# Kernel optimization log

Hardware: AMD Instinct MI355X
Metric: run time of the kernel (lower is better)

The kernel has to match this reference:

```python
import jax, jax.numpy as jnp
import numpy as np

DIM, HEADS, HEAD_DIM = 1024, 16, 64
B, S = 2, 1024
LAMBDA = 4.0
EPS = 1e-6


def setup_inputs() -> dict:
    key = jax.random.key(0)
    ks = jax.random.split(key, 7)
    sc = 1.0 / np.sqrt(DIM)
    return {
        "x": jax.random.normal(ks[0], (B, S, DIM), jnp.float32),
        "qkv_w": jax.random.normal(ks[1], (3 * DIM, DIM), jnp.float32) * sc,
        "qkv_b": jax.random.normal(ks[2], (3 * DIM,), jnp.float32) * 0.01,
        "proj_w": jax.random.normal(ks[3], (DIM, DIM), jnp.float32) * sc,
        "proj_b": jax.random.normal(ks[4], (DIM,), jnp.float32) * 0.01,
        "dwc_w": jax.random.normal(ks[5], (DIM, 1, 3), jnp.float32) * 0.3,
        "dwc_b": jax.random.normal(ks[6], (DIM,), jnp.float32) * 0.01,
    }


def _l1_dist(q, k):
    # q,k: [B,H,S,Dh] -> pairwise L1 distance [B,H,S,S].
    # Accumulate over head_dim with a (rematerialized) scan so we never
    # materialize the [B,H,S,S,Dh] broadcast tensor.
    qT = jnp.moveaxis(q, -1, 0)  # [Dh,B,H,S]
    kT = jnp.moveaxis(k, -1, 0)

    def step(acc, qk):
        qd, kd = qk  # [B,H,S]
        return acc + jnp.abs(qd[..., :, None] - kd[..., None, :]), None

    init = jnp.zeros(q.shape[:-1] + (k.shape[-2],), q.dtype)
    dist, _ = jax.lax.scan(jax.checkpoint(step), init, (qT, kT))
    return dist


def reference(x, qkv_w, qkv_b, proj_w, proj_b, dwc_w, dwc_b):
    Bq, Sq, C = x.shape
    # qkv projection -> q,k,v each [B,H,S,Dh]
    qkv = (x @ qkv_w.T + qkv_b).reshape(Bq, Sq, 3, HEADS, HEAD_DIM)
    qkv = jnp.transpose(qkv, (2, 0, 3, 1, 4))
    q, k, v = qkv[0], qkv[1], qkv[2]

    # exact Laplacian (L1-distance) kernel attention, row-normalized
    dist = _l1_dist(q, k)                       # [B,H,S,S]
    kern = jnp.exp(-LAMBDA * dist / HEAD_DIM)   # mean-L1 scaling
    attn = kern / (jnp.sum(kern, axis=-1, keepdims=True) + EPS)
    global_attn = jnp.einsum("bhij,bhjd->bhid", attn, v)

    # depthwise conv1d local branch on v (channel order = head-major)
    v1d = jnp.transpose(v, (0, 1, 3, 2)).reshape(Bq, C, Sq)  # [B,C,S]
    local = jax.lax.conv_general_dilated(
        v1d, dwc_w, window_strides=(1,), padding=((1, 1),),
        feature_group_count=C, dimension_numbers=("NCH", "OIH", "NCH"))
    local = local + dwc_b[None, :, None]
    local = jnp.transpose(local.reshape(Bq, HEADS, HEAD_DIM, Sq), (0, 1, 3, 2))

    y = global_attn + local                      # [B,H,S,Dh]
    y = jnp.transpose(y, (0, 2, 1, 3)).reshape(Bq, Sq, C)
    return y @ proj_w.T + proj_b
```

## Files before the change

### kernel.cpp

```cpp
#include <hip/hip_runtime.h>

#define DIMC 1024
#define HEADS 16
#define HD 64
#define BATCH 2
#define SEQ 1024
#define NQKV 3072

typedef _Float16 f16;
typedef _Float16 half8 __attribute__((ext_vector_type(8)));
typedef _Float16 half4v __attribute__((ext_vector_type(4)));
typedef float floatx4 __attribute__((ext_vector_type(4)));

__device__ __forceinline__ void gld16(const void* g, void* l) {
  __builtin_amdgcn_global_load_lds((const __attribute__((address_space(1))) void*)g,
                                   (__attribute__((address_space(3))) void*)l, 16, 0, 0);
}

__device__ __forceinline__ unsigned sadU8(unsigned a, unsigned b, unsigned c) {
#if __has_builtin(__builtin_amdgcn_sad_u8)
  return __builtin_amdgcn_sad_u8(a, b, c);
#else
  unsigned d;
  asm("v_sad_u8 %0, %1, %2, %3" : "=v"(d) : "v"(a), "v"(b), "v"(c));
  return d;
#endif
}

__global__ __launch_bounds__(256) void cvt_kernel(
    const float* __restrict__ x, const float* __restrict__ wq, const float* __restrict__ wp,
    f16* __restrict__ x16, f16* __restrict__ wq16, f16* __restrict__ wp16)
{
  int bid = blockIdx.x;
  const float* src; f16* dst; int base;
  if (bid < 512)        { src = x;  dst = x16;  base = bid; }
  else if (bid < 1280)  { src = wq; dst = wq16; base = bid - 512; }
  else                  { src = wp; dst = wp16; base = bid - 1280; }
  long long i0 = (long long)base*1024 + threadIdx.x;
#pragma unroll
  for (int k2 = 0; k2 < 4; ++k2) {
    long long i = i0 + k2*256;
    float4 v = ((const float4*)src)[i];
    half4v h; h[0]=(f16)v.x; h[1]=(f16)v.y; h[2]=(f16)v.z; h[3]=(f16)v.w;
    *(half4v*)(dst + i*4) = h;
  }
}

template<int TM, int TN, int BK, int MW, int MODE>
__global__ __launch_bounds__(256, MW) void gemm_kernel(
    const f16* __restrict__ A, const f16* __restrict__ Bw, const float* __restrict__ bias,
    unsigned char* __restrict__ q8, unsigned char* __restrict__ k8, f16* __restrict__ vT,
    float* __restrict__ outp, int K)
{
  constexpr int MT = TM / 32;
  constexpr int NT = TN / 32;
  constexpr int G  = BK / 8;
  __shared__ f16 As[TM*BK];
  __shared__ f16 Bs[TN*BK];
  const int tid = threadIdx.x;
  const int wave = tid >> 6, lane = tid & 63;
  const int lq = lane >> 4, li = lane & 15;
  const int m0 = blockIdx.y * TM, n0 = blockIdx.x * TN;
  const int wm = (wave & 1) * (TM/2), wn = (wave >> 1) * (TN/2);
  floatx4 acc[MT][NT] = {};

  const int kIters = K / BK;
  for (int kt = 0; kt < kIters; ++kt) {
    __syncthreads();
#pragma unroll
    for (int r = 0; r < TM*BK/2048; ++r) {
      int slot = r*256 + tid;
      int row = slot / G, c = slot % G, g = c ^ (row & (G-1));
      gld16(A + (size_t)(m0+row)*K + kt*BK + g*8, As + slot*8);
    }
#pragma unroll
    for (int r = 0; r < TN*BK/2048; ++r) {
      int slot = r*256 + tid;
      int row = slot / G, c = slot % G, g = c ^ (row & (G-1));
      gld16(Bw + (size_t)(n0+row)*K + kt*BK + g*8, Bs + slot*8);
    }
    __syncthreads();
#pragma unroll
    for (int ks = 0; ks < BK/32; ++ks) {
      half8 af[MT], bf[NT];
      int kc = ks*4 + lq;
#pragma unroll
      for (int t = 0; t < MT; ++t) {
        int am = wm + t*16 + li;
        af[t] = *(const half8*)&As[am*BK + (kc ^ (am & (G-1)))*8];
      }
#pragma unroll
      for (int t = 0; t < NT; ++t) {
        int bn = wn + t*16 + li;
        bf[t] = *(const half8*)&Bs[bn*BK + (kc ^ (bn & (G-1)))*8];
      }
#pragma unroll
      for (int mt = 0; mt < MT; ++mt)
#pragma unroll
        for (int nt = 0; nt < NT; ++nt)
          acc[mt][nt] = __builtin_amdgcn_mfma_f32_16x16x32_f16(af[mt], bf[nt], acc[mt][nt], 0, 0, 0);
    }
  }

#pragma unroll
  for (int mt = 0; mt < MT; ++mt) {
#pragma unroll
    for (int nt = 0; nt < NT; ++nt) {
      int f = n0 + wn + nt*16 + li;
      float bb = bias[f];
      if (MODE == 0) {
        int which = f >> 10, cc = f & 1023, h = cc >> 6, d = cc & 63;
        int t0 = m0 + wm + mt*16 + lq*4;
        int b = t0 >> 10, s0 = t0 & 1023;
        if (which == 2) {
          half4v hv;
#pragma unroll
          for (int r = 0; r < 4; ++r) hv[r] = (f16)(acc[mt][nt][r] + bb);
          *(half4v*)&vT[((size_t)((b*HEADS + h)*HD + d))*SEQ + s0] = hv;
        } else {
          unsigned char* dst = (which == 0) ? q8 : k8;
#pragma unroll
          for (int r = 0; r < 4; ++r) {
            float v = acc[mt][nt][r] + bb;
            int u = (int)floorf(v * 16.0f + 128.5f);
            u = u < 0 ? 0 : (u > 255 ? 255 : u);
            dst[((size_t)((b*HEADS + h)*SEQ + s0 + r))*HD + d] = (unsigned char)u;
          }
        }
      } else {
#pragma unroll
        for (int r = 0; r < 4; ++r) {
          int t = m0 + wm + mt*16 + lq*4 + r;
          outp[(size_t)t*DIMC + f] = acc[mt][nt][r] + bb;
        }
      }
    }
  }
}

__global__ __launch_bounds__(256, 4) void attn_kernel(
    const unsigned char* __restrict__ q8g, const unsigned char* __restrict__ k8g,
    const f16* __restrict__ vTg, const float* __restrict__ dwcw, const float* __restrict__ dwcb,
    f16* __restrict__ y16)
{
  __shared__ unsigned char q8s[32*64];
  __shared__ unsigned char k8s[2][128*64];
  __shared__ f16 sfrag[2][8*64*8];
  __shared__ float rspart[32*16];
  __shared__ float rowsum[32];

  const int tid = threadIdx.x;
  const int lin = blockIdx.x + 16 * blockIdx.y;
  const int bh = (lin & 7) * 4 + ((lin >> 3) & 3);
  const int i0 = (lin >> 5) * 32;
  const int lane = tid & 63, wave = tid >> 6;
  const int lq = lane >> 4, li = lane & 15;
  const int iL = tid & 15, jt = tid >> 4;
  const int ksj = jt >> 2, qj = jt & 3;
  const int scs = jt & 3;

  {
    if (tid < 128)
      gld16(q8g + ((size_t)(bh*SEQ) + i0)*HD + tid*16, q8s + tid*16);
#pragma unroll
    for (int r = 0; r < 2; ++r) {
      int slot = r*256 + tid;
      int row = slot >> 2, c4 = slot & 3, sc4 = c4 ^ ((row >> 3) & 3);
      gld16(k8g + ((size_t)(bh*SEQ) + row)*HD + sc4*16, k8s[0] + slot*16);
    }
  }
  __syncthreads();

  unsigned qr[2][16];
#pragma unroll
  for (int n = 0; n < 2; ++n)
#pragma unroll
    for (int c4 = 0; c4 < 4; ++c4) {
      uint4 t = *(const uint4*)&q8s[(iL + n*16)*64 + c4*16];
      qr[n][c4*4+0] = t.x; qr[n][c4*4+1] = t.y; qr[n][c4*4+2] = t.z; qr[n][c4*4+3] = t.w;
    }

  float rs[2] = {0.f, 0.f};
  floatx4 pacc[2] = {};
  const f16* vbase = vTg + ((size_t)(bh*HD) + wave*16 + li)*SEQ;

  for (int jb = 0; jb < 8; ++jb) {
    const int j0 = jb * 128;
    const int cur = jb & 1;

    if (jb < 7) {
#pragma unroll
      for (int r = 0; r < 2; ++r) {
        int slot = r*256 + tid;
        int row = slot >> 2, c4 = slot & 3, sc4 = c4 ^ ((row >> 3) & 3);
        gld16(k8g + ((size_t)(bh*SEQ) + j0 + 128 + row)*HD + sc4*16,
              k8s[cur ^ 1] + slot*16);
      }
    }
    half8 vfrag[4];
#pragma unroll
    for (int ks = 0; ks < 4; ++ks)
      vfrag[ks] = *(const half8*)(vbase + j0 + (ks*4 + lq)*8);

    unsigned sacc[2][8] = {};
#pragma unroll
    for (int c4 = 0; c4 < 4; ++c4) {
      uint4 kk[8];
#pragma unroll
      for (int jj = 0; jj < 8; ++jj)
        kk[jj] = *(const uint4*)&k8s[cur][(jt*8 + jj)*64 + ((c4 ^ scs) << 4)];
#pragma unroll
      for (int n = 0; n < 2; ++n)
#pragma unroll
        for (int jj = 0; jj < 8; ++jj) {
          sacc[n][jj] = sadU8(qr[n][c4*4+0], kk[jj].x, sacc[n][jj]);
          sacc[n][jj] = sadU8(qr[n][c4*4+1], kk[jj].y, sacc[n][jj]);
          sacc[n][jj] = sadU8(qr[n][c4*4+2], kk[jj].z, sacc[n][jj]);
          sacc[n][jj] = sadU8(qr[n][c4*4+3], kk[jj].w, sacc[n][jj]);
        }
    }
#pragma unroll
    for (int n = 0; n < 2; ++n) {
      half8 sv;
#pragma unroll
      for (int jj = 0; jj < 8; ++jj) {
        float sf = exp2f(-0.0056355275f * (float)sacc[n][jj]);
        rs[n] += sf;
        sv[jj] = (f16)sf;
      }
      *(half8*)&sfrag[cur][((n*4 + ksj)*64 + qj*16 + iL)*8] = sv;
    }
    __syncthreads();

#pragma unroll
    for (int ks = 0; ks < 4; ++ks) {
      half8 a0 = *(const half8*)&sfrag[cur][((0*4 + ks)*64 + lane)*8];
      half8 a1 = *(const half8*)&sfrag[cur][((1*4 + ks)*64 + lane)*8];
      pacc[0] = __builtin_amdgcn_mfma_f32_16x16x32_f16(a0, vfrag[ks], pacc[0], 0, 0, 0);
      pacc[1] = __builtin_amdgcn_mfma_f32_16x16x32_f16(a1, vfrag[ks], pacc[1], 0, 0, 0);
    }
  }

#pragma unroll
  for (int n = 0; n < 2; ++n) rspart[(iL + n*16)*16 + jt] = rs[n];
  __syncthreads();
  if (tid < 32) {
    float s = 0.f;
#pragma unroll
    for (int t = 0; t < 16; ++t) s += rspart[tid*16 + t];
    rowsum[tid] = s + 1e-6f;
  }
  __syncthreads();

  const int b = bh >> 4, h = bh & 15;
  {
    int d = wave*16 + li;
    int c = h*64 + d;
    float w0 = dwcw[c*3+0], w1 = dwcw[c*3+1], w2 = dwcw[c*3+2], cb = dwcb[c];
    const f16* vrow = vTg + ((size_t)(bh*HD) + d)*SEQ;
#pragma unroll
    for (int mt = 0; mt < 2; ++mt) {
      int s0 = i0 + mt*16 + lq*4;
      float vv[6];
#pragma unroll
      for (int e = 0; e < 6; ++e) {
        int s = s0 - 1 + e;
        vv[e] = (s >= 0 && s < SEQ) ? (float)vrow[s] : 0.f;
      }
#pragma unroll
      for (int r = 0; r < 4; ++r) {
        int ii = mt*16 + lq*4 + r;
        float val = pacc[mt][r] / rowsum[ii];
        val += w0*vv[r] + w1*vv[r+1] + w2*vv[r+2] + cb;
        int s = i0 + ii;
        y16[((size_t)(b*SEQ + s))*DIMC + c] = (f16)val;
      }
    }
  }
}

extern "C" void kernel_launch(void* const* d_in, const int* in_sizes, int n_in,
                              void* d_out, int out_size, void* d_ws, size_t ws_size,
                              hipStream_t stream) {
  const float* x      = (const float*)d_in[0];
  const float* qkv_w  = (const float*)d_in[1];
  const float* qkv_b  = (const float*)d_in[2];
  const float* proj_w = (const float*)d_in[3];
  const float* proj_b = (const float*)d_in[4];
  const float* dwc_w  = (const float*)d_in[5];
  const float* dwc_b  = (const float*)d_in[6];
  float* out = (float*)d_out;

  char* ws = (char*)d_ws;
  f16* x16  = (f16*)(ws);
  f16* wq16 = (f16*)(ws + (4ll<<20));
  f16* wp16 = (f16*)(ws + (10ll<<20));
  unsigned char* q8 = (unsigned char*)(ws + (12ll<<20));
  unsigned char* k8 = (unsigned char*)(ws + (14ll<<20));
  f16* vT   = (f16*)(ws + (16ll<<20));
  f16* y16  = (f16*)(ws + (20ll<<20));

  cvt_kernel<<<1536, 256, 0, stream>>>(x, qkv_w, proj_w, x16, wq16, wp16);
  gemm_kernel<128,128,128,2,0><<<dim3(24, 16), 256, 0, stream>>>(x16, wq16, qkv_b, q8, k8, vT, nullptr, DIMC);
  attn_kernel<<<dim3(16, 64), 256, 0, stream>>>(q8, k8, vT, dwc_w, dwc_b, y16);
  gemm_kernel<64,64,128,4,1><<<dim3(16, 32), 256, 0, stream>>>(y16, wp16, proj_b, nullptr, nullptr, nullptr, out, DIMC);
}
```

Before: 146.5 us.

## Feed SAD scores directly into MFMA from registers, reduce partial PV across waves

The attention kernel no longer writes the f16 exponentiated scores to shared memory and reads them back as MFMA A-operands. Each wave multiplies its own score fragment by V fragments covering all 64 head dims, accumulating per-wave partial PV results over its subset of keys. The four partials are summed through a shared-memory reduction in the epilogue, which also rewrites the depthwise-conv output with vectorized stores. This removes per-iteration LDS traffic but quadruples accumulator registers, so launch bounds drop from 4 to 3 blocks per SM.

```diff
diff --git a/kernel.cpp b/kernel.cpp
--- a/kernel.cpp
+++ b/kernel.cpp
@@ -138,14 +138,14 @@
   }
 }
 
-__global__ __launch_bounds__(256, 4) void attn_kernel(
+__global__ __launch_bounds__(256, 3) void attn_kernel(
     const unsigned char* __restrict__ q8g, const unsigned char* __restrict__ k8g,
     const f16* __restrict__ vTg, const float* __restrict__ dwcw, const float* __restrict__ dwcb,
     f16* __restrict__ y16)
 {
   __shared__ unsigned char q8s[32*64];
   __shared__ unsigned char k8s[2][128*64];
-  __shared__ f16 sfrag[2][8*64*8];
+  __shared__ float red[4][16][64];
   __shared__ float rspart[32*16];
   __shared__ float rowsum[32];
 
@@ -156,7 +156,6 @@
   const int lane = tid & 63, wave = tid >> 6;
   const int lq = lane >> 4, li = lane & 15;
   const int iL = tid & 15, jt = tid >> 4;
-  const int ksj = jt >> 2, qj = jt & 3;
   const int scs = jt & 3;
 
   {
@@ -181,8 +180,8 @@
     }
 
   float rs[2] = {0.f, 0.f};
-  floatx4 pacc[2] = {};
-  const f16* vbase = vTg + ((size_t)(bh*HD) + wave*16 + li)*SEQ;
+  floatx4 pacc[2][4] = {};
+  const int jw = wave*32 + lq*8;
 
   for (int jb = 0; jb < 8; ++jb) {
     const int j0 = jb * 128;
@@ -199,8 +198,8 @@
     }
     half8 vfrag[4];
 #pragma unroll
-    for (int ks = 0; ks < 4; ++ks)
-      vfrag[ks] = *(const half8*)(vbase + j0 + (ks*4 + lq)*8);
+    for (int dt = 0; dt < 4; ++dt)
+      vfrag[dt] = *(const half8*)(vTg + ((size_t)(bh*HD) + dt*16 + li)*SEQ + j0 + jw);
 
     unsigned sacc[2][8] = {};
 #pragma unroll
@@ -228,17 +227,11 @@
         rs[n] += sf;
         sv[jj] = (f16)sf;
       }
-      *(half8*)&sfrag[cur][((n*4 + ksj)*64 + qj*16 + iL)*8] = sv;
+#pragma unroll
+      for (int dt = 0; dt < 4; ++dt)
+        pacc[n][dt] = __builtin_amdgcn_mfma_f32_16x16x32_f16(sv, vfrag[dt], pacc[n][dt], 0, 0, 0);
     }
     __syncthreads();
-
-#pragma unroll
-    for (int ks = 0; ks < 4; ++ks) {
-      half8 a0 = *(const half8*)&sfrag[cur][((0*4 + ks)*64 + lane)*8];
-      half8 a1 = *(const half8*)&sfrag[cur][((1*4 + ks)*64 + lane)*8];
-      pacc[0] = __builtin_amdgcn_mfma_f32_16x16x32_f16(a0, vfrag[ks], pacc[0], 0, 0, 0);
-      pacc[1] = __builtin_amdgcn_mfma_f32_16x16x32_f16(a1, vfrag[ks], pacc[1], 0, 0, 0);
-    }
   }
 
 #pragma unroll
@@ -253,29 +246,39 @@
   __syncthreads();
 
   const int b = bh >> 4, h = bh & 15;
-  {
-    int d = wave*16 + li;
-    int c = h*64 + d;
-    float w0 = dwcw[c*3+0], w1 = dwcw[c*3+1], w2 = dwcw[c*3+2], cb = dwcb[c];
-    const f16* vrow = vTg + ((size_t)(bh*HD) + d)*SEQ;
-#pragma unroll
-    for (int mt = 0; mt < 2; ++mt) {
-      int s0 = i0 + mt*16 + lq*4;
-      float vv[6];
-#pragma unroll
-      for (int e = 0; e < 6; ++e) {
-        int s = s0 - 1 + e;
-        vv[e] = (s >= 0 && s < SEQ) ? (float)vrow[s] : 0.f;
-      }
-#pragma unroll
-      for (int r = 0; r < 4; ++r) {
-        int ii = mt*16 + lq*4 + r;
-        float val = pacc[mt][r] / rowsum[ii];
-        val += w0*vv[r] + w1*vv[r+1] + w2*vv[r+2] + cb;
-        int s = i0 + ii;
-        y16[((size_t)(b*SEQ + s))*DIMC + c] = (f16)val;
-      }
-    }
+  const int ie = tid >> 4, d40 = (tid & 15) * 4;
+#pragma unroll
+  for (int half = 0; half < 2; ++half) {
+#pragma unroll
+    for (int dt = 0; dt < 4; ++dt)
+#pragma unroll
+      for (int r = 0; r < 4; ++r)
+        red[wave][lq*4 + r][dt*16 + li] = pacc[half][dt][r];
+    __syncthreads();
+    float4 s = make_float4(0.f, 0.f, 0.f, 0.f);
+#pragma unroll
+    for (int w = 0; w < 4; ++w) {
+      float4 t = *(const float4*)&red[w][ie][d40];
+      s.x += t.x; s.y += t.y; s.z += t.z; s.w += t.w;
+    }
+    int srow = i0 + half*16 + ie;
+    float rsum = rowsum[half*16 + ie];
+    float sa[4] = {s.x, s.y, s.z, s.w};
+    half4v outv;
+#pragma unroll
+    for (int c = 0; c < 4; ++c) {
+      int d = d40 + c;
+      int ch = h*64 + d;
+      const f16* vrow = vTg + ((size_t)(bh*HD) + d)*SEQ;
+      float vm1 = (srow - 1 >= 0) ? (float)vrow[srow - 1] : 0.f;
+      float v0  = (float)vrow[srow];
+      float vp1 = (srow + 1 < SEQ) ? (float)vrow[srow + 1] : 0.f;
+      float val = sa[c] / rsum
+                + dwcw[ch*3+0]*vm1 + dwcw[ch*3+1]*v0 + dwcw[ch*3+2]*vp1 + dwcb[ch];
+      outv[c] = (f16)val;
+    }
+    *(half4v*)&y16[((size_t)(b*SEQ + srow))*DIMC + h*64 + d40] = outv;
+    if (half == 0) __syncthreads();
   }
 }
 
```

After: 152.4 us. +4.1%, slower.
